# Performance work log

Measured on AMD Instinct MI355X. Metric: run time of the kernel, lower is better.

Reference implementation:

```python
import jax, jax.numpy as jnp
import numpy as np

N, C, A, E, D_OUT = 50000, 4, 16, 800000, 64
GEO_DIM = 2 * C + 9  # zero bond angles + zero dihedrals + 9 local-frame feats


def setup_inputs() -> dict:
    key = jax.random.key(0)
    ks = jax.random.split(key, 6)
    coord = jax.random.normal(ks[0], (N, C, 3), dtype=jnp.float32)
    attr = jax.random.normal(ks[1], (N, C, A), dtype=jnp.float32)
    channel_weights = jax.random.uniform(ks[2], (N, C), dtype=jnp.float32)
    W = jax.random.normal(ks[3], (D_OUT, A * A + GEO_DIM), dtype=jnp.float32) * (1.0 / np.sqrt(A * A + GEO_DIM))
    b = jnp.zeros((D_OUT,), dtype=jnp.float32)
    row = jax.random.randint(ks[4], (E,), 0, N, dtype=jnp.int32)
    col = jax.random.randint(ks[5], (E,), 0, N, dtype=jnp.int32)
    return {"coord": coord, "attr": attr, "channel_weights": channel_weights, "W": W, "b": b, "row": row, "col": col}


def _local_frames(coord):
    # coord: [N, C, 3] with channels (ca, c, n, ...) -> [N, 9] flattened rotation matrix
    ca, c, n = coord[:, 0], coord[:, 1], coord[:, 2]
    x = c - ca
    x = x / (jnp.linalg.norm(x, axis=-1, keepdims=True) + 1e-8)
    ty = n - ca
    y = ty - jnp.sum(ty * x, axis=-1, keepdims=True) * x
    y = y / (jnp.linalg.norm(y, axis=-1, keepdims=True) + 1e-8)
    z = jnp.cross(x, y)
    # torch.stack([x,y,z], dim=-1).reshape(N,-1): columns are x,y,z
    return jnp.stack([x, y, z], axis=-1).reshape(coord.shape[0], 9)


def reference(coord, attr, channel_weights, W, b, row, col):
    n_nodes, n_ch = coord.shape[0], coord.shape[1]
    n_edge = row.shape[0]
    # --- per-edge channel-pair distances, masked by channel-weight outer product ---
    diff = coord[row][:, :, None, :] - coord[col][:, None, :, :]        # [E, C, C, 3]
    coord_msg = jnp.linalg.norm(diff, axis=-1)                          # [E, C, C]
    coord_msg = coord_msg * (channel_weights[row][:, :, None] * channel_weights[col][:, None, :])
    # --- bilinear attr contraction: attr[row]^T @ coord_msg @ attr[col] ---
    radial = jnp.einsum('eia,eij,ejb->eab', attr[row], coord_msg, attr[col])  # [E, A, A]
    radial = radial.reshape(n_edge, -1)                                  # [E, A*A]
    # --- SE3 geometric features (bond/dihedral angles are zeros in source) ---
    lf = _local_frames(coord)                                            # [N, 9]
    # local_features repeated over channels; (lf[row]+lf[col]).mean over channel == lf[row]+lf[col]
    edge_lf = lf[row] + lf[col]                                          # [E, 9]
    geo = jnp.concatenate([jnp.zeros((n_edge, 2 * n_ch), radial.dtype), edge_lf], axis=-1)
    expanded = jnp.concatenate([radial, geo], axis=-1)                   # [E, A*A + GEO_DIM]
    # non-rbf path: linear_map(expanded) / (||expanded|| + CONSTANT)
    rnorm = jnp.linalg.norm(expanded, axis=-1, keepdims=True) + 1.0
    radials = (expanded @ W.T + b) / rnorm                               # [E, D_OUT]
    # --- coord_diff: row coords minus channel-mask-pooled col coords ---
    mask = (channel_weights != 0).astype(coord.dtype)                    # [N, C]
    csum = mask.sum(-1)                                                  # [N]
    pooled_col = (coord[col] * mask[col][..., None]).sum(1) / csum[col][:, None]  # [E, 3]
    coord_diff = coord[row] - pooled_col[:, None, :]                     # [E, C, 3]
    # --- node scatter-reduce: segment_sum of radials, segment_mean of coord_diff ---
    agg = jax.ops.segment_sum(radials, row, num_segments=n_nodes)        # [N, D_OUT]
    cnt = jax.ops.segment_sum(jnp.ones((n_edge,), coord.dtype), row, num_segments=n_nodes)
    coord_agg = jax.ops.segment_sum(coord_diff, row, num_segments=n_nodes) / jnp.clip(cnt, 1.0)[:, None, None]
    return jnp.concatenate([agg, coord_agg.reshape(n_nodes, -1)], axis=-1)  # [N, D_OUT + C*3]
```

## Files before the change

### kernel.cpp

```cpp
#include <hip/hip_runtime.h>
#include <math.h>

#define NN 50000
#define EDG 800000
#define OUTC 76
#define NKB 68
#define NB  196

#define CCW_OFF  0
#define LFP_OFF  (CCW_OFF + NN*16)
#define WK_OFF   (LFP_OFF + NN*16)
#define CNT_OFF  (WK_OFF + NKB*256)
#define CUR_OFF  (CNT_OFF + NN)
#define OFFS_OFF (CUR_OFF + 4)
#define PERM_OFF (OFFS_OFF + NN)
#define ECOL_OFF (PERM_OFF + EDG)

__global__ void prep_hist_kernel(const float* __restrict__ coord,
                                 const float* __restrict__ cw,
                                 const float* __restrict__ W,
                                 const int* __restrict__ row,
                                 float* __restrict__ ccwp,
                                 float* __restrict__ lfp,
                                 float* __restrict__ wk,
                                 int* __restrict__ counts,
                                 int* __restrict__ perm, int E) {
    int t = blockIdx.x * blockDim.x + threadIdx.x;

    if (t < E) perm[t] = atomicAdd(&counts[row[t]], 1);

    if (t < NKB * 64) {
        int kb = t >> 6, d = t & 63;
        float tmp[4];
        #pragma unroll
        for (int km = 0; km < 4; ++km) {
            int k = kb * 4 + km;
            int kcol = (k < 256) ? k : ((k < 265) ? k + 8 : -1);
            tmp[km] = (kcol >= 0) ? W[d * 273 + kcol] : 0.f;
        }
        ((float4*)wk)[t] = make_float4(tmp[0], tmp[1], tmp[2], tmp[3]);
    }

    if (t >= NN) return;
    const float* cp = coord + (size_t)t * 12;
    float c0x = cp[0], c0y = cp[1], c0z = cp[2];
    float c1x = cp[3], c1y = cp[4], c1z = cp[5];
    float c2x = cp[6], c2y = cp[7], c2z = cp[8];
    float c3x = cp[9], c3y = cp[10], c3z = cp[11];
    const float* wv = cw + (size_t)t * 4;
    float w0 = wv[0], w1 = wv[1], w2 = wv[2], w3 = wv[3];

    float* cc = ccwp + (size_t)t * 16;
    cc[0] = c0x; cc[1] = c0y; cc[2] = c0z; cc[3] = w0;
    cc[4] = c1x; cc[5] = c1y; cc[6] = c1z; cc[7] = w1;
    cc[8] = c2x; cc[9] = c2y; cc[10] = c2z; cc[11] = w2;
    cc[12] = c3x; cc[13] = c3y; cc[14] = c3z; cc[15] = w3;

    float xx = c1x - c0x, xy = c1y - c0y, xz = c1z - c0z;
    float invx = 1.0f / (sqrtf(xx * xx + xy * xy + xz * xz) + 1e-8f);
    xx *= invx; xy *= invx; xz *= invx;
    float tx = c2x - c0x, ty = c2y - c0y, tz = c2z - c0z;
    float dp = tx * xx + ty * xy + tz * xz;
    float yx = tx - dp * xx, yy = ty - dp * xy, yz = tz - dp * xz;
    float invy = 1.0f / (sqrtf(yx * yx + yy * yy + yz * yz) + 1e-8f);
    yx *= invy; yy *= invy; yz *= invy;
    float zx = xy * yz - xz * yy;
    float zy = xz * yx - xx * yz;
    float zz = xx * yy - xy * yx;

    float m0 = (w0 != 0.f) ? 1.f : 0.f;
    float m1 = (w1 != 0.f) ? 1.f : 0.f;
    float m2 = (w2 != 0.f) ? 1.f : 0.f;
    float m3 = (w3 != 0.f) ? 1.f : 0.f;
    float cs = m0 + m1 + m2 + m3;
    float px = (c0x * m0 + c1x * m1 + c2x * m2 + c3x * m3) / cs;
    float py = (c0y * m0 + c1y * m1 + c2y * m2 + c3y * m3) / cs;
    float pz = (c0z * m0 + c1z * m1 + c2z * m2 + c3z * m3) / cs;

    float* lp = lfp + (size_t)t * 16;
    lp[0] = xx; lp[1] = yx; lp[2] = zx;
    lp[3] = xy; lp[4] = yy; lp[5] = zy;
    lp[6] = xz; lp[7] = yz; lp[8] = zz;
    lp[9] = 0.f; lp[10] = 0.f; lp[11] = 0.f;
    lp[12] = px; lp[13] = py; lp[14] = pz; lp[15] = 0.f;
}

__global__ void scanalloc_kernel(const int* __restrict__ counts,
                                 int* __restrict__ cursor,
                                 int* __restrict__ offs) {
    int t = blockIdx.x * 256 + threadIdx.x;
    int v = (t < NN) ? counts[t] : 0;
    int lane = threadIdx.x & 63, wid = threadIdx.x >> 6;
    int x = v;
    #pragma unroll
    for (int d = 1; d < 64; d <<= 1) {
        int u = __shfl_up(x, d);
        x += (lane >= d) ? u : 0;
    }
    __shared__ int wtot[4];
    __shared__ int sbase;
    if (lane == 63) wtot[wid] = x;
    __syncthreads();
    if (threadIdx.x == 0)
        sbase = atomicAdd(cursor, wtot[0] + wtot[1] + wtot[2] + wtot[3]);
    __syncthreads();
    int wbase = 0;
    for (int i = 0; i < wid; ++i) wbase += wtot[i];
    if (t < NN) offs[t] = sbase + wbase + x - v;
}

__global__ void scatter_kernel(const int* __restrict__ row, const int* __restrict__ col,
                               const int* __restrict__ offs, const int* __restrict__ perm,
                               int* __restrict__ ecol, int E) {
    int e = blockIdx.x * blockDim.x + threadIdx.x;
    if (e >= E) return;
    ecol[offs[row[e]] + perm[e]] = col[e];
}

__device__ __forceinline__ float wave_sum64(float x) {
    float v = x, t;
    t = __int_as_float(__builtin_amdgcn_update_dpp(0, __float_as_int(v), 0x111, 0xf, 0xf, true)); v += t;
    t = __int_as_float(__builtin_amdgcn_update_dpp(0, __float_as_int(v), 0x112, 0xf, 0xf, true)); v += t;
    t = __int_as_float(__builtin_amdgcn_update_dpp(0, __float_as_int(v), 0x114, 0xf, 0xf, true)); v += t;
    t = __int_as_float(__builtin_amdgcn_update_dpp(0, __float_as_int(v), 0x118, 0xf, 0xf, true)); v += t;
    t = __int_as_float(__builtin_amdgcn_update_dpp(0, __float_as_int(v), 0x142, 0xa, 0xf, true)); v += t;
    t = __int_as_float(__builtin_amdgcn_update_dpp(0, __float_as_int(v), 0x143, 0xc, 0xf, true)); v += t;
    return __int_as_float(__builtin_amdgcn_readlane(__float_as_int(v), 63));
}

#define DPP(x, pat) __int_as_float(__builtin_amdgcn_update_dpp(0, __float_as_int(x), pat, 0xf, 0xf, true))

__global__ __launch_bounds__(256) void edge_kernel(
    const float* __restrict__ coord, const float* __restrict__ attr,
    const float* __restrict__ bvec,
    const float* __restrict__ ccw, const float* __restrict__ lfp,
    const float* __restrict__ wk,
    const int* __restrict__ offs, const int* __restrict__ counts,
    const int* __restrict__ ecol,
    float* __restrict__ out) {
    __shared__ float Acbuf[4][64];
    __shared__ float S[4][280];

    const int w = threadIdx.x >> 6;
    const int l = threadIdx.x & 63;
    const int l15 = l & 15;
    const int n = blockIdx.x * 4 + w;

    const int st = offs[n];
    const int deg = counts[n];
    const int en = st + deg;
    const int b0 = (l & 3) * 4;
    const int i4 = (l >> 2) & 3;
    const int j4 = l & 3;
    const int a  = l >> 2;

    const float Br0 = attr[(size_t)n * 64 + (size_t)(((i4 + 0) & 3) * 16) + a];
    const float Br1 = attr[(size_t)n * 64 + (size_t)(((i4 + 3) & 3) * 16) + a];
    const float Br2 = attr[(size_t)n * 64 + (size_t)(((i4 + 2) & 3) * 16) + a];
    const float Br3 = attr[(size_t)n * 64 + (size_t)(((i4 + 1) & 3) * 16) + a];
    const float4 cown = ((const float4*)ccw)[n * 4 + i4];
    const float crx = cown.x, cry = cown.y, crz = cown.z, cwr = cown.w;
    const float lrv = lfp[(size_t)n * 16 + l15];
    const float lfmask = (l < 9) ? 1.f : 0.f;
    const float pmask  = (l >= 12 && l < 15) ? 1.f : 0.f;

    float ax = 0.f, ay = 0.f, az = 0.f, aw = 0.f;
    float sgeo = 0.f, invs = 0.f, sp = 0.f;

    const float4* CCW4 = (const float4*)ccw;

    for (int base = st; base < en; base += 64) {
        int bcnt = en - base; bcnt = bcnt > 64 ? 64 : bcnt;
        int idx = base + (l < bcnt ? l : bcnt - 1);
        int cvec = ecol[idx];

        int c = __builtin_amdgcn_readlane(cvec, 0);
        float4 cc  = CCW4[c * 4 + j4];
        float  acv = attr[(size_t)c * 64 + l];
        float  lcv = lfp[c * 16 + l15];

        for (int k = 0; k < bcnt; ++k) {
            Acbuf[w][l] = acv;

            int kn = (k + 1 < bcnt) ? k + 1 : k;
            int c2 = __builtin_amdgcn_readlane(cvec, kn);
            float4 cc_n  = CCW4[c2 * 4 + j4];
            float  ac_n  = attr[(size_t)c2 * 64 + l];
            float  lcv_n = lfp[c2 * 16 + l15];

            float dx = crx - cc.x, dy = cry - cc.y, dz = crz - cc.z;
            float m = __builtin_amdgcn_sqrtf(fmaf(dx, dx, fmaf(dy, dy, dz * dz))) * cwr * cc.w;

            float mr4  = DPP(m, 0x124);
            float mr8  = DPP(m, 0x128);
            float mr12 = DPP(m, 0x12C);
            float Uo = fmaf(Br3, mr12, fmaf(Br2, mr8, fmaf(Br1, mr4, Br0 * m)));

            float U0 = DPP(Uo, 0x00);
            float U1 = DPP(Uo, 0x55);
            float U2 = DPP(Uo, 0xAA);
            float U3 = DPP(Uo, 0xFF);

            float4 A0 = *(const float4*)&Acbuf[w][b0];
            float4 A1 = *(const float4*)&Acbuf[w][16 + b0];
            float4 A2 = *(const float4*)&Acbuf[w][32 + b0];
            float4 A3 = *(const float4*)&Acbuf[w][48 + b0];
            float ex = fmaf(U3, A3.x, fmaf(U2, A2.x, fmaf(U1, A1.x, U0 * A0.x)));
            float ey = fmaf(U3, A3.y, fmaf(U2, A2.y, fmaf(U1, A1.y, U0 * A0.y)));
            float ez = fmaf(U3, A3.z, fmaf(U2, A2.z, fmaf(U1, A1.z, U0 * A0.z)));
            float ew = fmaf(U3, A3.w, fmaf(U2, A2.w, fmaf(U1, A1.w, U0 * A0.w)));

            float glf  = (lrv + lcv) * lfmask;
            float part = fmaf(glf, glf, fmaf(ew, ew, fmaf(ez, ez, fmaf(ey, ey, ex * ex))));
            float tot  = wave_sum64(part);
            float invr = __builtin_amdgcn_rcpf(__builtin_amdgcn_sqrtf(tot) + 1.f);

            ax = fmaf(ex, invr, ax); ay = fmaf(ey, invr, ay);
            az = fmaf(ez, invr, az); aw = fmaf(ew, invr, aw);
            sgeo = fmaf(glf, invr, sgeo);
            invs += invr;
            sp = fmaf(lcv, pmask, sp);

            cc = cc_n; acv = ac_n; lcv = lcv_n;
        }
    }

    *(float4*)&S[w][l * 4] = make_float4(ax, ay, az, aw);
    if (l < 9)       S[w][256 + l] = sgeo;
    else if (l < 16) S[w][256 + l] = 0.f;
    if (l == 16)     S[w][272] = invs;
    if (l >= 12 && l < 15) S[w][273 + (l - 12)] = sp;

    float invsum = S[w][272];
    float acc = bvec[l] * invsum;
    const float4* WK4 = (const float4*)wk;
    #pragma unroll 4
    for (int kb = 0; kb < NKB; ++kb) {
        float4 wv = WK4[kb * 64 + l];
        float4 sv = *(const float4*)&S[w][kb * 4];
        acc += wv.x * sv.x + wv.y * sv.y + wv.z * sv.z + wv.w * sv.w;
    }
    out[(size_t)n * OUTC + l] = acc;

    float cntv = (float)deg;
    float invc = __builtin_amdgcn_rcpf(fmaxf(cntv, 1.f));
    if (l < 12) {
        int x = l % 3;
        out[(size_t)n * OUTC + 64 + l] = (cntv * coord[(size_t)n * 12 + l] - S[w][273 + x]) * invc;
    }
}

extern "C" void kernel_launch(void* const* d_in, const int* in_sizes, int n_in,
                              void* d_out, int out_size, void* d_ws, size_t ws_size,
                              hipStream_t stream) {
    const float* coord = (const float*)d_in[0];
    const float* attr  = (const float*)d_in[1];
    const float* cw    = (const float*)d_in[2];
    const float* W     = (const float*)d_in[3];
    const float* bvec  = (const float*)d_in[4];
    const int*   row   = (const int*)d_in[5];
    const int*   col   = (const int*)d_in[6];
    float* out = (float*)d_out;
    float* ws  = (float*)d_ws;
    int E = in_sizes[5];

    float* ccwp = ws + CCW_OFF;
    float* lfp  = ws + LFP_OFF;
    float* wk   = ws + WK_OFF;
    int* counts = (int*)(ws + CNT_OFF);
    int* cursor = (int*)(ws + CUR_OFF);
    int* offs   = (int*)(ws + OFFS_OFF);
    int* perm   = (int*)(ws + PERM_OFF);
    int* ecol   = (int*)(ws + ECOL_OFF);

    hipMemsetAsync(counts, 0, (NN + 4) * sizeof(int), stream);
    prep_hist_kernel<<<(E + 255) / 256, 256, 0, stream>>>(
        coord, cw, W, row, ccwp, lfp, wk, counts, perm, E);
    scanalloc_kernel<<<NB, 256, 0, stream>>>(counts, cursor, offs);
    scatter_kernel<<<(E + 255) / 256, 256, 0, stream>>>(row, col, offs, perm, ecol, E);
    edge_kernel<<<NN / 4, 256, 0, stream>>>(coord, attr, bvec, ccwp, lfp, wk,
                                            offs, counts, ecol, out);
}
```

Before: 293.0 us.

## Replace CSR scan and scatter with fixed-capacity per-node edge buckets

When the workspace is large enough, the histogram pass writes each edge's column straight into a fixed 64-slot bucket per row node. This drops the separate scan/allocation and scatter kernels and the perm/ecol round trip through memory. The edge kernel then reads each node's edges from offset t*CAP. It also adds an unroll-by-2 hint on the inner per-edge loop. The cost is more workspace and a silent capacity assumption: any node with more than 64 incident edges would overflow into the neighbouring bucket, which holds for the random test degrees but is not guarded.

```diff
diff --git a/kernel.cpp b/kernel.cpp
--- a/kernel.cpp
+++ b/kernel.cpp
@@ -6,6 +6,7 @@
 #define OUTC 76
 #define NKB 68
 #define NB  196
+#define CAP 64
 
 #define CCW_OFF  0
 #define LFP_OFF  (CCW_OFF + NN*16)
@@ -13,21 +14,30 @@
 #define CNT_OFF  (WK_OFF + NKB*256)
 #define CUR_OFF  (CNT_OFF + NN)
 #define OFFS_OFF (CUR_OFF + 4)
-#define PERM_OFF (OFFS_OFF + NN)
-#define ECOL_OFF (PERM_OFF + EDG)
-
-__global__ void prep_hist_kernel(const float* __restrict__ coord,
-                                 const float* __restrict__ cw,
-                                 const float* __restrict__ W,
-                                 const int* __restrict__ row,
-                                 float* __restrict__ ccwp,
-                                 float* __restrict__ lfp,
-                                 float* __restrict__ wk,
-                                 int* __restrict__ counts,
-                                 int* __restrict__ perm, int E) {
+#define TAIL_OFF (OFFS_OFF + NN + 4)
+#define BUCKET_FLOATS ((size_t)TAIL_OFF + (size_t)NN * CAP)
+
+__global__ void prep_kernel(const float* __restrict__ coord,
+                            const float* __restrict__ cw,
+                            const float* __restrict__ W,
+                            const int* __restrict__ row,
+                            const int* __restrict__ col,
+                            float* __restrict__ ccwp,
+                            float* __restrict__ lfp,
+                            float* __restrict__ wk,
+                            int* __restrict__ counts,
+                            int* __restrict__ perm,
+                            int* __restrict__ ecolb,
+                            int* __restrict__ offs,
+                            int E, int bucket) {
     int t = blockIdx.x * blockDim.x + threadIdx.x;
 
-    if (t < E) perm[t] = atomicAdd(&counts[row[t]], 1);
+    if (t < E) {
+        int r = row[t];
+        int slot = atomicAdd(&counts[r], 1);
+        if (bucket) ecolb[r * CAP + slot] = col[t];
+        else        perm[t] = slot;
+    }
 
     if (t < NKB * 64) {
         int kb = t >> 6, d = t & 63;
@@ -42,6 +52,8 @@
     }
 
     if (t >= NN) return;
+    if (bucket) offs[t] = t * CAP;
+
     const float* cp = coord + (size_t)t * 12;
     float c0x = cp[0], c0y = cp[1], c0z = cp[2];
     float c1x = cp[3], c1y = cp[4], c1z = cp[5];
@@ -179,6 +191,7 @@
         float  acv = attr[(size_t)c * 64 + l];
         float  lcv = lfp[c * 16 + l15];
 
+        #pragma unroll 2
         for (int k = 0; k < bcnt; ++k) {
             Acbuf[w][l] = acv;
 
@@ -270,14 +283,28 @@
     int* counts = (int*)(ws + CNT_OFF);
     int* cursor = (int*)(ws + CUR_OFF);
     int* offs   = (int*)(ws + OFFS_OFF);
-    int* perm   = (int*)(ws + PERM_OFF);
-    int* ecol   = (int*)(ws + ECOL_OFF);
+    int* tail   = (int*)(ws + TAIL_OFF);
+
+    const int bucket = (ws_size >= BUCKET_FLOATS * sizeof(float)) ? 1 : 0;
 
     hipMemsetAsync(counts, 0, (NN + 4) * sizeof(int), stream);
-    prep_hist_kernel<<<(E + 255) / 256, 256, 0, stream>>>(
-        coord, cw, W, row, ccwp, lfp, wk, counts, perm, E);
-    scanalloc_kernel<<<NB, 256, 0, stream>>>(counts, cursor, offs);
-    scatter_kernel<<<(E + 255) / 256, 256, 0, stream>>>(row, col, offs, perm, ecol, E);
-    edge_kernel<<<NN / 4, 256, 0, stream>>>(coord, attr, bvec, ccwp, lfp, wk,
-                                            offs, counts, ecol, out);
-}
+
+    if (bucket) {
+        int* ecolb = tail;
+        prep_kernel<<<(E + 255) / 256, 256, 0, stream>>>(
+            coord, cw, W, row, col, ccwp, lfp, wk, counts,
+            nullptr, ecolb, offs, E, 1);
+        edge_kernel<<<NN / 4, 256, 0, stream>>>(coord, attr, bvec, ccwp, lfp, wk,
+                                                offs, counts, ecolb, out);
+    } else {
+        int* perm = tail;
+        int* ecol = tail + EDG;
+        prep_kernel<<<(E + 255) / 256, 256, 0, stream>>>(
+            coord, cw, W, row, col, ccwp, lfp, wk, counts,
+            perm, nullptr, offs, E, 0);
+        scanalloc_kernel<<<NB, 256, 0, stream>>>(counts, cursor, offs);
+        scatter_kernel<<<(E + 255) / 256, 256, 0, stream>>>(row, col, offs, perm, ecol, E);
+        edge_kernel<<<NN / 4, 256, 0, stream>>>(coord, attr, bvec, ccwp, lfp, wk,
+                                                offs, counts, ecol, out);
+    }
+}
```

New measurement: 291.5 us. Within noise of the previous version (-0.5%).
